# Kernel tuning notes

Measured on AMD Instinct MI355X. Metric: run time of the kernel, lower is better.

Reference implementation:

```python
import jax, jax.numpy as jnp
import numpy as np

B, S, D, H = 2, 2048, 1024, 16
DH = D // H  # head_dim = 64


def setup_inputs() -> dict:
    key = jax.random.key(0)
    ks = jax.random.split(key, 10)
    inp = {
        "query": jax.random.normal(ks[0], (B, S, D), jnp.float32),
        "key": jax.random.normal(ks[1], (B, S, D), jnp.float32),
        "value": jax.random.normal(ks[2], (B, S, D), jnp.float32),
        "mask": jnp.ones((B, S), jnp.int32),
        # per-head q/k/v projections stacked over the head axis [H, D, DH]
        "Wq": jax.random.normal(ks[3], (H, D, DH), jnp.float32) * 0.02,
        "bq": jnp.zeros((H, DH), jnp.float32),
        "Wk": jax.random.normal(ks[4], (H, D, DH), jnp.float32) * 0.02,
        "bk": jnp.zeros((H, DH), jnp.float32),
        "Wv": jax.random.normal(ks[5], (H, D, DH), jnp.float32) * 0.02,
        "bv": jnp.zeros((H, DH), jnp.float32),
        # output projection fc: Linear(D, D)
        "Wo": jax.random.normal(ks[6], (D, D), jnp.float32) * 0.02,
        "bo": jnp.zeros((D,), jnp.float32),
    }
    return inp


def reference(query, key, value, mask, Wq, bq, Wk, bk, Wv, bv, Wo, bo):
    scale = 1.0 / jnp.sqrt(jnp.asarray(DH, query.dtype))
    # batched per-head projections: [B,S,D] x [H,D,DH] -> [B,H,S,DH]
    q = jnp.einsum('bsd,hde->bhse', query, Wq) + bq[None, :, None, :]
    k = jnp.einsum('bsd,hde->bhse', key, Wk) + bk[None, :, None, :]
    v = jnp.einsum('bsd,hde->bhse', value, Wv) + bv[None, :, None, :]
    # scaled dot-product attention scores [B,H,Sq,Sk]
    scores = jnp.einsum('bhqe,bhke->bhqk', q, k) * scale
    scores = jnp.where(mask[:, None, None, :] == 0, jnp.asarray(-1e9, scores.dtype), scores)
    attn = jax.nn.softmax(scores, axis=-1)
    ctx = jnp.einsum('bhqk,bhke->bhqe', attn, v)          # [B,H,S,DH]
    ctx = ctx.transpose(0, 2, 1, 3).reshape(query.shape[0], -1, H * DH)  # concat heads
    return ctx @ Wo + bo
```

## Files before the change

kernel.cpp:

```cpp
#include <hip/hip_runtime.h>
#include <stdint.h>
#include <math.h>


typedef __attribute__((ext_vector_type(8))) short short8;
typedef __attribute__((ext_vector_type(4))) short short4v;
typedef __attribute__((ext_vector_type(4))) float floatx4;

#define LOG2E 1.44269504088896340736f

__device__ __forceinline__ unsigned short f32_bf16(float f) {
  union { float f; unsigned u; } c; c.f = f;
  return (unsigned short)((c.u + 0x7FFFu + ((c.u >> 16) & 1u)) >> 16);
}
__device__ __forceinline__ float bf16_f32(unsigned short u) {
  union { unsigned u; float f; } c; c.u = ((unsigned)u) << 16;
  return c.f;
}
__device__ __forceinline__ void gld16(const void* g, void* l) {
  __builtin_amdgcn_global_load_lds((const __attribute__((address_space(1))) void*)g,
                                   (__attribute__((address_space(3))) void*)l, 16, 0, 0);
}


__global__ __launch_bounds__(256) void prep_kernel(
    const float* __restrict__ qf, const float* __restrict__ kf, const float* __restrict__ vf,
    const float* __restrict__ w0, const float* __restrict__ w1, const float* __restrict__ w2,
    const float* __restrict__ wo, const int* __restrict__ mask,
    unsigned short* __restrict__ oq, unsigned short* __restrict__ ok, unsigned short* __restrict__ ov,
    unsigned short* __restrict__ o0, unsigned short* __restrict__ o1, unsigned short* __restrict__ o2,
    unsigned short* __restrict__ oo, float* __restrict__ mb) {
  __shared__ float t[32][33];
  const int y = blockIdx.y, bx = blockIdx.x;
  if (y < 3) {
    if (y == 0 && bx < 16) {
      int j = bx * 256 + threadIdx.x;
      mb[j] = (mask[j] == 0) ? (-1.0e9f * LOG2E) : 0.0f;
    }
    const float* in = (y == 0) ? qf : (y == 1) ? kf : vf;
    unsigned short* out = (y == 0) ? oq : (y == 1) ? ok : ov;
    int i = bx * 256 + threadIdx.x;
    float4 v = reinterpret_cast<const float4*>(in)[i];
    ushort4 o;
    o.x = f32_bf16(v.x); o.y = f32_bf16(v.y); o.z = f32_bf16(v.z); o.w = f32_bf16(v.w);
    reinterpret_cast<ushort4*>(out)[i] = o;
    return;
  }
  const int tx = threadIdx.x & 31, ty = threadIdx.x >> 5;
  const float* in; unsigned short* out; int R, C, z, r0, c0;
  if (bx < 3072) {
    const int zb = bx >> 6, rem = bx & 63;
    const int sel = zb >> 4; z = zb & 15;
    in = (sel == 0) ? w0 : (sel == 1) ? w1 : w2;
    out = (sel == 0) ? o0 : (sel == 1) ? o1 : o2;
    R = 1024; C = 64; r0 = (rem >> 1) * 32; c0 = (rem & 1) * 32;
  } else {
    const int t2 = bx - 3072;
    in = wo; out = oo; R = 1024; C = 1024; z = 0;
    r0 = (t2 >> 5) * 32; c0 = (t2 & 31) * 32;
  }
  const float* inp = in + (size_t)z * R * C;
  #pragma unroll
  for (int j = 0; j < 4; ++j)
    t[ty + j * 8][tx] = inp[(size_t)(r0 + ty + j * 8) * C + c0 + tx];
  __syncthreads();
  #pragma unroll
  for (int j = 0; j < 4; ++j)
    out[((size_t)z * C + c0 + ty + j * 8) * R + r0 + tx] = f32_bf16(t[tx][ty + j * 8]);
}


__global__ __launch_bounds__(512, 2) void gemm_proj_kernel(
    const unsigned short* __restrict__ qin, const unsigned short* __restrict__ kin,
    const unsigned short* __restrict__ vin,
    const unsigned short* __restrict__ WqT, const unsigned short* __restrict__ WkT,
    const unsigned short* __restrict__ WvT,
    const float* __restrict__ bq, const float* __restrict__ bk, const float* __restrict__ bv,
    unsigned short* __restrict__ Qp, unsigned short* __restrict__ Kp,
    unsigned short* __restrict__ Vt) {
  __shared__ unsigned short As[2][2][128 * 64];
  __shared__ unsigned short Bs[2][2][128 * 64];

  const int z = blockIdx.y;
  const int x = blockIdx.x;
  const int r = x & 7, q = x >> 3;
  int mt, nt;
  if (z < 2) { mt = r * 2 + (q >> 2); nt = q & 3; }
  else       { nt = r * 2 + (q >> 2); mt = q & 3; }
  const int blockM = mt * 256, blockN = nt * 256;

  const unsigned short* A  = (z == 0) ? qin : (z == 1) ? kin : WvT;
  const unsigned short* Bt = (z == 0) ? WqT : (z == 1) ? WkT : vin;
  const float* bias = (z == 0) ? bq : (z == 1) ? bk : bv;

  const int tid = threadIdx.x;
  const int w = tid >> 6, lane = tid & 63;
  const int quad = lane >> 4, l15 = lane & 15;
  const int wm = w & 1, wn = w >> 1;

  const int lr8 = lane >> 3;
  const int lc8 = lane & 7;
  const int gcs = lc8 ^ lr8;

  auto stage = [&](int k0, int buf) {
    #pragma unroll
    for (int h = 0; h < 2; ++h)
      #pragma unroll
      for (int s2 = 0; s2 < 2; ++s2) {
        const int rl = s2 * 64 + w * 8;
        gld16(A + (size_t)(blockM + h * 128 + rl + lr8) * 1024 + k0 + gcs * 8,
              &As[buf][h][rl * 64]);
      }
    #pragma unroll
    for (int h = 0; h < 2; ++h)
      #pragma unroll
      for (int s2 = 0; s2 < 2; ++s2) {
        const int rl = s2 * 64 + w * 8;
        gld16(Bt + (size_t)(blockN + h * 128 + rl + lr8) * 1024 + k0 + gcs * 8,
              &Bs[buf][h][rl * 64]);
      }
  };

  floatx4 acc[8][4];
  #pragma unroll
  for (int mi = 0; mi < 8; ++mi)
    #pragma unroll
    for (int ni = 0; ni < 4; ++ni)
      acc[mi][ni] = (floatx4){0.f, 0.f, 0.f, 0.f};

  stage(0, 0);
  __syncthreads();

  const int brb = (wn & 1) * 64;

  for (int st = 0; st < 16; ++st) {
    const int buf = st & 1;
    const unsigned short* Ah = &As[buf][wm][0];
    const unsigned short* Bh = &Bs[buf][wn >> 1][0];
    short8 af[4][2], b0[2][2], b1[2][2];

    if (st + 1 < 16) stage((st + 1) * 64, buf ^ 1);
    #pragma unroll
    for (int mi = 0; mi < 4; ++mi) {
      const int row = mi * 16 + l15;
      #pragma unroll
      for (int kk = 0; kk < 2; ++kk)
        af[mi][kk] = *(const short8*)(Ah + row * 64 + (((kk * 4 + quad) ^ (row & 7)) << 3));
    }
    #pragma unroll
    for (int ni = 0; ni < 2; ++ni) {
      const int row = brb + ni * 16 + l15;
      #pragma unroll
      for (int kk = 0; kk < 2; ++kk)
        b0[ni][kk] = *(const short8*)(Bh + row * 64 + (((kk * 4 + quad) ^ (row & 7)) << 3));
    }
    __builtin_amdgcn_s_barrier();
    __builtin_amdgcn_s_setprio(1);
    #pragma unroll
    for (int mi = 0; mi < 4; ++mi)
      #pragma unroll
      for (int ni = 0; ni < 2; ++ni)
        #pragma unroll
        for (int kk = 0; kk < 2; ++kk)
          acc[mi][ni] = __builtin_amdgcn_mfma_f32_16x16x32_bf16(af[mi][kk], b0[ni][kk], acc[mi][ni], 0, 0, 0);
    __builtin_amdgcn_s_setprio(0);
    __builtin_amdgcn_s_barrier();

    #pragma unroll
    for (int ni = 0; ni < 2; ++ni) {
      const int row = brb + (ni + 2) * 16 + l15;
      #pragma unroll
      for (int kk = 0; kk < 2; ++kk)
        b1[ni][kk] = *(const short8*)(Bh + row * 64 + (((kk * 4 + quad) ^ (row & 7)) << 3));
    }
    __builtin_amdgcn_s_barrier();
    __builtin_amdgcn_s_setprio(1);
    #pragma unroll
    for (int mi = 0; mi < 4; ++mi)
      #pragma unroll
      for (int ni = 0; ni < 2; ++ni)
        #pragma unroll
        for (int kk = 0; kk < 2; ++kk)
          acc[mi][ni + 2] = __builtin_amdgcn_mfma_f32_16x16x32_bf16(af[mi][kk], b1[ni][kk], acc[mi][ni + 2], 0, 0, 0);
    __builtin_amdgcn_s_setprio(0);
    __builtin_amdgcn_s_barrier();

    #pragma unroll
    for (int mi = 0; mi < 4; ++mi) {
      const int row = (mi + 4) * 16 + l15;
      #pragma unroll
      for (int kk = 0; kk < 2; ++kk)
        af[mi][kk] = *(const short8*)(Ah + row * 64 + (((kk * 4 + quad) ^ (row & 7)) << 3));
    }
    __builtin_amdgcn_s_barrier();
    __builtin_amdgcn_s_setprio(1);
    #pragma unroll
    for (int mi = 0; mi < 4; ++mi)
      #pragma unroll
      for (int ni = 0; ni < 2; ++ni)
        #pragma unroll
        for (int kk = 0; kk < 2; ++kk)
          acc[mi + 4][ni + 2] = __builtin_amdgcn_mfma_f32_16x16x32_bf16(af[mi][kk], b1[ni][kk], acc[mi + 4][ni + 2], 0, 0, 0);
    __builtin_amdgcn_s_setprio(0);
    __builtin_amdgcn_s_barrier();

    __builtin_amdgcn_s_setprio(1);
    #pragma unroll
    for (int mi = 0; mi < 4; ++mi)
      #pragma unroll
      for (int ni = 0; ni < 2; ++ni)
        #pragma unroll
        for (int kk = 0; kk < 2; ++kk)
          acc[mi + 4][ni] = __builtin_amdgcn_mfma_f32_16x16x32_bf16(af[mi][kk], b0[ni][kk], acc[mi + 4][ni], 0, 0, 0);
    __builtin_amdgcn_s_setprio(0);
    __syncthreads();
  }

  unsigned short* Cw = (w < 4) ? ((unsigned short*)As + w * 8192)
                               : ((unsigned short*)Bs + (w - 4) * 8192);
  const int pc = lc8 ^ lr8;

  if (z < 2) {
    unsigned short* outp = z ? Kp : Qp;
    const int n0 = blockN + wn * 64;
    const int m0 = blockM + wm * 128;
    float bn[4];
    #pragma unroll
    for (int ni = 0; ni < 4; ++ni) bn[ni] = bias[n0 + ni * 16 + l15];
    #pragma unroll
    for (int mi = 0; mi < 8; ++mi)
      #pragma unroll
      for (int ni = 0; ni < 4; ++ni)
        #pragma unroll
        for (int rr = 0; rr < 4; ++rr) {
          const int row = mi * 16 + quad * 4 + rr;
          const int col = ni * 16 + l15;
          Cw[row * 64 + (((col >> 3) ^ (row & 7)) << 3) + (col & 7)] =
              f32_bf16(acc[mi][ni][rr] + bn[ni]);
        }
    const size_t bb = (size_t)(m0 >> 11);
    const int h = n0 >> 6, s0 = m0 & 2047;
    unsigned short* dst = outp + ((bb * 16 + h) * 2048 + s0) * 64;
    #pragma unroll
    for (int ps = 0; ps < 16; ++ps) {
      const int lr = ps * 8 + lr8;
      *(short8*)(dst + lr * 64 + lc8 * 8) = *(const short8*)(Cw + lr * 64 + pc * 8);
    }
  } else {
    const int m0 = blockM + wm * 128;
    const int n0 = blockN + wn * 64;
    #pragma unroll
    for (int mi = 0; mi < 8; ++mi) {
      float bm[4];
      #pragma unroll
      for (int rr = 0; rr < 4; ++rr) bm[rr] = bias[m0 + mi * 16 + quad * 4 + rr];
      #pragma unroll
      for (int ni = 0; ni < 4; ++ni)
        #pragma unroll
        for (int rr = 0; rr < 4; ++rr) {
          const int row = mi * 16 + quad * 4 + rr;
          const int col = ni * 16 + l15;
          Cw[row * 64 + (((col >> 3) ^ (row & 7)) << 3) + (col & 7)] =
              f32_bf16(acc[mi][ni][rr] + bm[rr]);
        }
    }
    const size_t bb = (size_t)(n0 >> 11);
    const int s0 = n0 & 2047;
    unsigned short* dst = Vt + (bb * 1024 + m0) * 2048 + s0;
    #pragma unroll
    for (int ps = 0; ps < 16; ++ps) {
      const int lr = ps * 8 + lr8;
      *(short8*)(dst + (size_t)lr * 2048 + lc8 * 8) = *(const short8*)(Cw + lr * 64 + pc * 8);
    }
  }
}


__global__ __launch_bounds__(256) void gemm_out_kernel(
    const unsigned short* __restrict__ A, const unsigned short* __restrict__ Bt,
    const float* __restrict__ bias, float* __restrict__ out, int K, int N) {
  __shared__ unsigned short As[2][128 * 64];
  __shared__ unsigned short Bs[2][64 * 64];
  const int tid = threadIdx.x;
  const int w = tid >> 6, lane = tid & 63;
  const int quad = lane >> 4, l15 = lane & 15;
  const int wm = w & 1, wn = w >> 1;
  const int lr8 = lane >> 3, lc8 = lane & 7;
  const int gcs = lc8 ^ lr8;
  const int l = blockIdx.x, r = l & 7, j = l >> 3;
  const int blockM = (r * 4 + (j & 3)) * 128;
  const int blockN = (j >> 2) * 64;

  floatx4 acc[4][2];
  #pragma unroll
  for (int mi = 0; mi < 4; ++mi)
    #pragma unroll
    for (int ni = 0; ni < 2; ++ni)
      acc[mi][ni] = (floatx4){0.f, 0.f, 0.f, 0.f};

  auto stage = [&](int k0, int buf) {
    #pragma unroll
    for (int i = 0; i < 4; ++i) {
      const int rl = w * 32 + i * 8;
      gld16(A + (size_t)(blockM + rl + lr8) * K + k0 + gcs * 8, As[buf] + rl * 64);
    }
    #pragma unroll
    for (int i = 0; i < 2; ++i) {
      const int rl = w * 16 + i * 8;
      gld16(Bt + (size_t)(blockN + rl + lr8) * K + k0 + gcs * 8, Bs[buf] + rl * 64);
    }
  };

  const int iters = K >> 6;
  stage(0, 0);
  for (int it = 0; it < iters; ++it) {
    __syncthreads();
    if (it + 1 < iters) stage((it + 1) * 64, (it + 1) & 1);
    const unsigned short* Asb = As[it & 1];
    const unsigned short* Bsb = Bs[it & 1];
    short8 bf[2][2];
    #pragma unroll
    for (int ni = 0; ni < 2; ++ni) {
      const int row = wn * 32 + ni * 16 + l15;
      #pragma unroll
      for (int kk = 0; kk < 2; ++kk)
        bf[ni][kk] = *(const short8*)(Bsb + row * 64 + (((kk * 4 + quad) ^ (row & 7)) << 3));
    }
    #pragma unroll
    for (int mi = 0; mi < 4; ++mi) {
      const int row = wm * 64 + mi * 16 + l15;
      #pragma unroll
      for (int kk = 0; kk < 2; ++kk) {
        short8 af = *(const short8*)(Asb + row * 64 + (((kk * 4 + quad) ^ (row & 7)) << 3));
        #pragma unroll
        for (int ni = 0; ni < 2; ++ni)
          acc[mi][ni] = __builtin_amdgcn_mfma_f32_16x16x32_bf16(af, bf[ni][kk], acc[mi][ni], 0, 0, 0);
      }
    }
  }

  #pragma unroll
  for (int mi = 0; mi < 4; ++mi)
    #pragma unroll
    for (int ni = 0; ni < 2; ++ni) {
      const int n = blockN + wn * 32 + ni * 16 + l15;
      const float bv = bias[n];
      #pragma unroll
      for (int rr = 0; rr < 4; ++rr) {
        const int m = blockM + wm * 64 + mi * 16 + quad * 4 + rr;
        out[(size_t)m * N + n] = acc[mi][ni][rr] + bv;
      }
    }
}


__global__ __launch_bounds__(256) void attn_kernel(
    const unsigned short* __restrict__ Q, const unsigned short* __restrict__ Kg,
    const unsigned short* __restrict__ Vt, const float* __restrict__ maskAdd,
    unsigned short* __restrict__ ctx) {
  const int S = 2048;
  const int tid = threadIdx.x;
  const int w = tid >> 6, lane = tid & 63, quad = lane >> 4, l15 = lane & 15;
  const int l = blockIdx.x, r8 = l & 7, j8 = l >> 3;
  const int bh = r8 * 4 + (j8 & 3);
  const int qb = j8 >> 2;
  const int b = bh >> 4, h = bh & 15;
  const int q0 = qb * 128;

  __shared__ unsigned short Ks[2][128 * 64];
  __shared__ unsigned short Vs[2][64 * 128];
  __shared__ unsigned short Ps[4][32 * 64];
  unsigned short* Pw = Ps[w];

  const unsigned short* Qb = Q + (size_t)bh * S * 64;
  const unsigned short* Kb = Kg + (size_t)bh * S * 64;
  const unsigned short* Vb = Vt + (size_t)bh * 64 * S;
  const float* mb = maskAdd + (size_t)b * S;

  const float qs = 0.125f * LOG2E;
  short8 qf[2][2];
  #pragma unroll
  for (int mi = 0; mi < 2; ++mi)
    #pragma unroll
    for (int kq = 0; kq < 2; ++kq) {
      short8 v = *(const short8*)(Qb + (size_t)(q0 + w * 32 + mi * 16 + l15) * 64 + kq * 32 + quad * 8);
      #pragma unroll
      for (int jj = 0; jj < 8; ++jj)
        v[jj] = (short)f32_bf16(bf16_f32((unsigned short)v[jj]) * qs);
      qf[mi][kq] = v;
    }

  floatx4 O[2][4];
  float lsum[2] = {0.f, 0.f};
  #pragma unroll
  for (int mi = 0; mi < 2; ++mi)
    #pragma unroll
    for (int ne = 0; ne < 4; ++ne) O[mi][ne] = (floatx4){0.f, 0.f, 0.f, 0.f};

  auto stage_kv = [&](int t, int buf) {
    const int kv0 = t * 128;
    #pragma unroll
    for (int i = 0; i < 4; ++i) {
      int r0 = w * 32 + i * 8;
      int row = r0 + (lane >> 3);
      int cg = (lane & 7) ^ (row & 7);
      gld16(Kb + (size_t)(kv0 + row) * 64 + cg * 8, Ks[buf] + r0 * 64);
    }
    #pragma unroll
    for (int i = 0; i < 4; ++i) {
      int r0 = w * 16 + i * 4;
      int row = r0 + (lane >> 4);
      int p = lane & 15;
      int cg = (p & 8) | ((p & 7) ^ (row & 7));
      gld16(Vb + (size_t)row * S + kv0 + cg * 8, Vs[buf] + r0 * 128);
    }
  };

  stage_kv(0, 0);
  for (int t = 0; t < 16; ++t) {
    const int kv0 = t * 128;
    __syncthreads();
    if (t + 1 < 16) stage_kv(t + 1, (t + 1) & 1);
    const unsigned short* Ksb = Ks[t & 1];
    const unsigned short* Vsb = Vs[t & 1];

    #pragma unroll
    for (int ph = 0; ph < 2; ++ph) {
      #pragma unroll
      for (int ni = 0; ni < 4; ++ni) {
        const int key16 = (ph * 4 + ni) * 16;
        short8 kf0 = *(const short8*)(Ksb + (key16 + l15) * 64 + ((quad ^ (l15 & 7)) * 8));
        short8 kf1 = *(const short8*)(Ksb + (key16 + l15) * 64 + (((4 + quad) ^ (l15 & 7)) * 8));
        const floatx4 m4 = *(const floatx4*)(mb + kv0 + key16 + quad * 4);
        #pragma unroll
        for (int mi = 0; mi < 2; ++mi) {
          floatx4 s = (floatx4){0.f, 0.f, 0.f, 0.f};
          s = __builtin_amdgcn_mfma_f32_16x16x32_bf16(kf0, qf[mi][0], s, 0, 0, 0);
          s = __builtin_amdgcn_mfma_f32_16x16x32_bf16(kf1, qf[mi][1], s, 0, 0, 0);
          short4v pk;
          #pragma unroll
          for (int rr = 0; rr < 4; ++rr) {
            const float p = __builtin_amdgcn_exp2f(s[rr] + m4[rr]);
            const unsigned short pb = f32_bf16(p);
            pk[rr] = (short)pb;
            lsum[mi] += bf16_f32(pb);
          }
          const int row = mi * 16 + l15;
          const int phys = (ni * 2 + (quad >> 1)) ^ (l15 & 7);
          *(short4v*)(Pw + row * 64 + phys * 8 + (quad & 1) * 4) = pk;
        }
      }
      asm volatile("" ::: "memory");
      #pragma unroll
      for (int kkl = 0; kkl < 2; ++kkl) {
        const int kk = ph * 2 + kkl;
        short8 pfr[2], vfr[4];
        #pragma unroll
        for (int mi = 0; mi < 2; ++mi)
          pfr[mi] = *(const short8*)(Pw + (mi * 16 + l15) * 64 + (((kkl * 4 + quad) ^ (l15 & 7)) << 3));
        #pragma unroll
        for (int ne = 0; ne < 4; ++ne) {
          const int c = kk * 4 + quad;
          vfr[ne] = *(const short8*)(Vsb + (ne * 16 + l15) * 128 + ((c & 8) | ((c & 7) ^ (l15 & 7))) * 8);
        }
        #pragma unroll
        for (int mi = 0; mi < 2; ++mi)
          #pragma unroll
          for (int ne = 0; ne < 4; ++ne)
            O[mi][ne] = __builtin_amdgcn_mfma_f32_16x16x32_bf16(pfr[mi], vfr[ne], O[mi][ne], 0, 0, 0);
      }
      asm volatile("" ::: "memory");
    }
  }

  #pragma unroll
  for (int mi = 0; mi < 2; ++mi) {
    float v = lsum[mi];
    v += __shfl_xor(v, 16);
    v += __shfl_xor(v, 32);
    #pragma unroll
    for (int rr = 0; rr < 4; ++rr) {
      const float lv = __shfl(v, quad * 4 + rr);
      const float inv = __builtin_amdgcn_rcpf(lv);
      const int s = q0 + w * 32 + mi * 16 + quad * 4 + rr;
      #pragma unroll
      for (int ne = 0; ne < 4; ++ne)
        ctx[((size_t)b * S + s) * 1024 + h * 64 + ne * 16 + l15] = f32_bf16(O[mi][ne][rr] * inv);
    }
  }
}


extern "C" void kernel_launch(void* const* d_in, const int* in_sizes, int n_in,
                              void* d_out, int out_size, void* d_ws, size_t ws_size,
                              hipStream_t stream) {
  const float* query = (const float*)d_in[0];
  const float* key   = (const float*)d_in[1];
  const float* value = (const float*)d_in[2];
  const int*   mask  = (const int*)d_in[3];
  const float* Wq = (const float*)d_in[4];
  const float* bq = (const float*)d_in[5];
  const float* Wk = (const float*)d_in[6];
  const float* bk = (const float*)d_in[7];
  const float* Wv = (const float*)d_in[8];
  const float* bv = (const float*)d_in[9];
  const float* Wo = (const float*)d_in[10];
  const float* bo = (const float*)d_in[11];
  float* out = (float*)d_out;

  char* ws = (char*)d_ws;
  const size_t MB = 1024 * 1024;
  unsigned short* qin  = (unsigned short*)(ws + 0);
  unsigned short* kin  = (unsigned short*)(ws + 8 * MB);
  unsigned short* vin  = (unsigned short*)(ws + 16 * MB);
  unsigned short* WqT  = (unsigned short*)(ws + 24 * MB);
  unsigned short* WkT  = (unsigned short*)(ws + 26 * MB);
  unsigned short* WvT  = (unsigned short*)(ws + 28 * MB);
  unsigned short* WoT  = (unsigned short*)(ws + 30 * MB);
  unsigned short* Qp   = (unsigned short*)(ws + 32 * MB);
  unsigned short* Kp   = (unsigned short*)(ws + 40 * MB);
  unsigned short* Vt   = (unsigned short*)(ws + 48 * MB);
  float* maskAdd       = (float*)(ws + 56 * MB);
  unsigned short* ctxb = qin;

  prep_kernel<<<dim3(4096, 4), 256, 0, stream>>>(query, key, value, Wq, Wk, Wv, Wo, mask,
                                                 qin, kin, vin, WqT, WkT, WvT, WoT, maskAdd);
  gemm_proj_kernel<<<dim3(64, 3), 512, 0, stream>>>(qin, kin, vin, WqT, WkT, WvT,
                                                    bq, bk, bv, Qp, Kp, Vt);
  attn_kernel<<<dim3(512), 256, 0, stream>>>(Qp, Kp, Vt, maskAdd, ctxb);
  gemm_out_kernel<<<dim3(512), 256, 0, stream>>>(ctxb, WoT, bo, out, 1024, 1024);
}
```

Before: 238.0 us.

## Shrink attention KV tile to 64 keys, pad P buffer, truncate bf16 rounding

The attention kernel now stages 64-key K/V tiles instead of 128-key tiles, running 32 iterations with a simpler single-phase loop per tile. This roughly halves LDS use, which could allow more resident blocks per CU. The P scratch buffer switches from an XOR swizzle to a padded row stride of 72. P is now converted to bf16 by truncation instead of round-to-nearest-even, which saves ALU work but slightly changes numerics. The smaller tiles double the number of barriers and staging steps.

```diff
diff --git a/kernel.cpp b/kernel.cpp
--- a/kernel.cpp
+++ b/kernel.cpp
@@ -367,9 +367,9 @@
   const int b = bh >> 4, h = bh & 15;
   const int q0 = qb * 128;
 
-  __shared__ unsigned short Ks[2][128 * 64];
-  __shared__ unsigned short Vs[2][64 * 128];
-  __shared__ unsigned short Ps[4][32 * 64];
+  __shared__ unsigned short Ks[2][64 * 64];
+  __shared__ unsigned short Vs[2][64 * 64];
+  __shared__ unsigned short Ps[4][32 * 72];
   unsigned short* Pw = Ps[w];
 
   const unsigned short* Qb = Q + (size_t)bh * S * 64;
@@ -398,79 +398,75 @@
     for (int ne = 0; ne < 4; ++ne) O[mi][ne] = (floatx4){0.f, 0.f, 0.f, 0.f};
 
   auto stage_kv = [&](int t, int buf) {
-    const int kv0 = t * 128;
-    #pragma unroll
-    for (int i = 0; i < 4; ++i) {
-      int r0 = w * 32 + i * 8;
+    const int kv0 = t * 64;
+    #pragma unroll
+    for (int i = 0; i < 2; ++i) {
+      int r0 = w * 16 + i * 8;
       int row = r0 + (lane >> 3);
       int cg = (lane & 7) ^ (row & 7);
       gld16(Kb + (size_t)(kv0 + row) * 64 + cg * 8, Ks[buf] + r0 * 64);
     }
     #pragma unroll
-    for (int i = 0; i < 4; ++i) {
-      int r0 = w * 16 + i * 4;
-      int row = r0 + (lane >> 4);
-      int p = lane & 15;
-      int cg = (p & 8) | ((p & 7) ^ (row & 7));
-      gld16(Vb + (size_t)row * S + kv0 + cg * 8, Vs[buf] + r0 * 128);
+    for (int i = 0; i < 2; ++i) {
+      int r0 = w * 16 + i * 8;
+      int row = r0 + (lane >> 3);
+      int cg = (lane & 7) ^ (row & 7);
+      gld16(Vb + (size_t)row * S + kv0 + cg * 8, Vs[buf] + r0 * 64);
     }
   };
 
   stage_kv(0, 0);
-  for (int t = 0; t < 16; ++t) {
-    const int kv0 = t * 128;
+  for (int t = 0; t < 32; ++t) {
+    const int kv0 = t * 64;
     __syncthreads();
-    if (t + 1 < 16) stage_kv(t + 1, (t + 1) & 1);
+    if (t + 1 < 32) stage_kv(t + 1, (t + 1) & 1);
     const unsigned short* Ksb = Ks[t & 1];
     const unsigned short* Vsb = Vs[t & 1];
 
     #pragma unroll
-    for (int ph = 0; ph < 2; ++ph) {
-      #pragma unroll
-      for (int ni = 0; ni < 4; ++ni) {
-        const int key16 = (ph * 4 + ni) * 16;
-        short8 kf0 = *(const short8*)(Ksb + (key16 + l15) * 64 + ((quad ^ (l15 & 7)) * 8));
-        short8 kf1 = *(const short8*)(Ksb + (key16 + l15) * 64 + (((4 + quad) ^ (l15 & 7)) * 8));
-        const floatx4 m4 = *(const floatx4*)(mb + kv0 + key16 + quad * 4);
-        #pragma unroll
-        for (int mi = 0; mi < 2; ++mi) {
-          floatx4 s = (floatx4){0.f, 0.f, 0.f, 0.f};
-          s = __builtin_amdgcn_mfma_f32_16x16x32_bf16(kf0, qf[mi][0], s, 0, 0, 0);
-          s = __builtin_amdgcn_mfma_f32_16x16x32_bf16(kf1, qf[mi][1], s, 0, 0, 0);
-          short4v pk;
-          #pragma unroll
-          for (int rr = 0; rr < 4; ++rr) {
-            const float p = __builtin_amdgcn_exp2f(s[rr] + m4[rr]);
-            const unsigned short pb = f32_bf16(p);
-            pk[rr] = (short)pb;
-            lsum[mi] += bf16_f32(pb);
-          }
-          const int row = mi * 16 + l15;
-          const int phys = (ni * 2 + (quad >> 1)) ^ (l15 & 7);
-          *(short4v*)(Pw + row * 64 + phys * 8 + (quad & 1) * 4) = pk;
+    for (int ni = 0; ni < 4; ++ni) {
+      const int key16 = ni * 16;
+      const int krow = key16 + l15;
+      short8 kf0 = *(const short8*)(Ksb + krow * 64 + ((quad ^ (l15 & 7)) * 8));
+      short8 kf1 = *(const short8*)(Ksb + krow * 64 + (((4 + quad) ^ (l15 & 7)) * 8));
+      const floatx4 m4 = *(const floatx4*)(mb + kv0 + key16 + quad * 4);
+      const int c = ni * 2 + (quad >> 1);
+      #pragma unroll
+      for (int mi = 0; mi < 2; ++mi) {
+        floatx4 s = (floatx4){0.f, 0.f, 0.f, 0.f};
+        s = __builtin_amdgcn_mfma_f32_16x16x32_bf16(kf0, qf[mi][0], s, 0, 0, 0);
+        s = __builtin_amdgcn_mfma_f32_16x16x32_bf16(kf1, qf[mi][1], s, 0, 0, 0);
+        short4v pk;
+        #pragma unroll
+        for (int rr = 0; rr < 4; ++rr) {
+          const float p = __builtin_amdgcn_exp2f(s[rr] + m4[rr]);
+          union { float f; unsigned u; } cc; cc.f = p;
+          pk[rr] = (short)(cc.u >> 16);
+          union { unsigned u; float f; } dd; dd.u = cc.u & 0xFFFF0000u;
+          lsum[mi] += dd.f;
         }
+        *(short4v*)(Pw + (mi * 16 + l15) * 72 + c * 8 + (quad & 1) * 4) = pk;
       }
-      asm volatile("" ::: "memory");
-      #pragma unroll
-      for (int kkl = 0; kkl < 2; ++kkl) {
-        const int kk = ph * 2 + kkl;
-        short8 pfr[2], vfr[4];
-        #pragma unroll
-        for (int mi = 0; mi < 2; ++mi)
-          pfr[mi] = *(const short8*)(Pw + (mi * 16 + l15) * 64 + (((kkl * 4 + quad) ^ (l15 & 7)) << 3));
-        #pragma unroll
-        for (int ne = 0; ne < 4; ++ne) {
-          const int c = kk * 4 + quad;
-          vfr[ne] = *(const short8*)(Vsb + (ne * 16 + l15) * 128 + ((c & 8) | ((c & 7) ^ (l15 & 7))) * 8);
-        }
-        #pragma unroll
-        for (int mi = 0; mi < 2; ++mi)
-          #pragma unroll
-          for (int ne = 0; ne < 4; ++ne)
-            O[mi][ne] = __builtin_amdgcn_mfma_f32_16x16x32_bf16(pfr[mi], vfr[ne], O[mi][ne], 0, 0, 0);
+    }
+    asm volatile("" ::: "memory");
+    #pragma unroll
+    for (int kkl = 0; kkl < 2; ++kkl) {
+      short8 pfr[2], vfr[4];
+      #pragma unroll
+      for (int mi = 0; mi < 2; ++mi)
+        pfr[mi] = *(const short8*)(Pw + (mi * 16 + l15) * 72 + (kkl * 4 + quad) * 8);
+      #pragma unroll
+      for (int ne = 0; ne < 4; ++ne) {
+        const int vrow = ne * 16 + l15;
+        vfr[ne] = *(const short8*)(Vsb + vrow * 64 + (((kkl * 4 + quad) ^ (l15 & 7)) * 8));
       }
-      asm volatile("" ::: "memory");
-    }
+      #pragma unroll
+      for (int mi = 0; mi < 2; ++mi)
+        #pragma unroll
+        for (int ne = 0; ne < 4; ++ne)
+          O[mi][ne] = __builtin_amdgcn_mfma_f32_16x16x32_bf16(pfr[mi], vfr[ne], O[mi][ne], 0, 0, 0);
+    }
+    asm volatile("" ::: "memory");
   }
 
   #pragma unroll
```

New measurement: 244.1 us. +2.6%, slower.
